# Performance work log

Measured on AMD Instinct MI355X. Metric: run time of the kernel, lower is better.

Reference implementation:

```python
import jax, jax.numpy as jnp
import numpy as np

D_MODEL = 1024
D_FF = 4096
NUM_EXPERTS = 8
NUM_SLOTS = 2
LN_EPS = 1e-5


def setup_inputs() -> dict:
    key = jax.random.key(0)
    ks = jax.random.split(key, 4)
    x = jax.random.normal(ks[0], (4, 4096, D_MODEL), dtype=jnp.float32)
    slot_embeds = jax.random.normal(ks[1], (NUM_EXPERTS * NUM_SLOTS, D_MODEL), dtype=jnp.float32) * 0.02
    # per-expert MLP weights, stacked over expert axis (Linear bias=False)
    W1 = jax.random.normal(ks[2], (NUM_EXPERTS, D_MODEL, D_FF), dtype=jnp.float32) * (1.0 / np.sqrt(D_MODEL))
    W2 = jax.random.normal(ks[3], (NUM_EXPERTS, D_FF, D_MODEL), dtype=jnp.float32) * (1.0 / np.sqrt(D_FF))
    ln_gamma = jnp.ones((D_MODEL,), dtype=jnp.float32)
    ln_beta = jnp.zeros((D_MODEL,), dtype=jnp.float32)
    return {"x": x, "slot_embeds": slot_embeds, "W1": W1, "W2": W2,
            "ln_gamma": ln_gamma, "ln_beta": ln_beta}


def reference(x, slot_embeds, W1, W2, ln_gamma, ln_beta):
    B, T, D = x.shape
    E, S = NUM_EXPERTS, NUM_SLOTS
    # logits: [B, T, E*S]
    logits = jnp.einsum('btd,nd->btn', x, slot_embeds) / jnp.sqrt(jnp.asarray(D, x.dtype))
    # dispatch: softmax over tokens (dim=1)
    dispatch = jax.nn.softmax(logits, axis=1)
    slot_in = jnp.einsum('btn,btd->bnd', dispatch, x)  # [B, E*S, D]
    # LayerNorm over last dim
    mu = jnp.mean(slot_in, axis=-1, keepdims=True)
    var = jnp.mean(jnp.square(slot_in - mu), axis=-1, keepdims=True)
    h = (slot_in - mu) * jax.lax.rsqrt(var + LN_EPS) * ln_gamma + ln_beta
    # per-expert MLP as a single batched (grouped) GEMM pair
    h = h.reshape(B, E, S, D)
    u = jax.nn.gelu(jnp.einsum('besd,edf->besf', h, W1), approximate=False)
    slot_out = jnp.einsum('besf,efd->besd', u, W2).reshape(B, E * S, D)
    # combine: softmax over slots (dim=2)
    combine = jax.nn.softmax(logits, axis=2)
    return jnp.einsum('btn,bnd->btd', combine, slot_out)
```

## Files before the change

### kernel.cpp

```cpp
#include <hip/hip_runtime.h>
#include <math.h>

#define NB 4
#define NT 4096
#define ND 1024
#define NS 16
#define NE 8
#define NF 4096

__device__ __forceinline__ float gelu(float v) {
  return 0.5f * v * (1.f + erff(v * 0.70710678118654752f));
}
__device__ __forceinline__ void fma4(float4& a, float s, const float4& v) {
  a.x += s * v.x; a.y += s * v.y; a.z += s * v.z; a.w += s * v.w;
}
__device__ __forceinline__ float4 ld4(const float* p) {
  return *reinterpret_cast<const float4*>(p);
}

__global__ __launch_bounds__(256, 4) void k_logits(const float* __restrict__ x,
                                                   const float* __restrict__ se,
                                                   float* __restrict__ logits) {
  const int wave = threadIdx.x >> 6, lane = threadIdx.x & 63;
  const int t0 = blockIdx.x * 16 + wave * 4;
  float acc[64];
#pragma unroll
  for (int j = 0; j < 64; ++j) acc[j] = 0.f;
  for (int it = 0; it < 4; ++it) {
    const int d = it * 256 + lane * 4;
    float4 xv[4];
#pragma unroll
    for (int tt = 0; tt < 4; ++tt)
      xv[tt] = ld4(x + (size_t)(t0 + tt) * ND + d);
#pragma unroll
    for (int n = 0; n < NS; ++n) {
      const float4 sv = ld4(se + (size_t)n * ND + d);
#pragma unroll
      for (int tt = 0; tt < 4; ++tt) {
        acc[tt * 16 + n] += xv[tt].x * sv.x + xv[tt].y * sv.y +
                            xv[tt].z * sv.z + xv[tt].w * sv.w;
      }
    }
  }
#pragma unroll
  for (int k = 0; k < 6; ++k) {
    const int dlt = 1 << k;
    const bool hi = (lane & dlt) != 0;
#pragma unroll
    for (int i = 0; i < (64 >> (k + 1)); ++i) {
      const float a = acc[2 * i], b = acc[2 * i + 1];
      const float send = hi ? a : b;
      const float recv = __shfl_xor(send, dlt, 64);
      acc[i] = (hi ? b : a) + recv;
    }
  }
  logits[(size_t)t0 * NS + lane] = acc[0] * 0.03125f;
}

__global__ __launch_bounds__(256) void k_softmax_stats(const float* __restrict__ logits,
                                                       float* __restrict__ stats) {
  int bn = blockIdx.x;
  int b = bn >> 4, n = bn & 15;
  __shared__ float red[256];
  const float* lp = logits + ((size_t)b * NT) * NS + n;
  float m = -1e30f;
  for (int t = threadIdx.x; t < NT; t += 256) m = fmaxf(m, lp[(size_t)t * NS]);
  red[threadIdx.x] = m; __syncthreads();
  for (int s = 128; s > 0; s >>= 1) {
    if (threadIdx.x < s) red[threadIdx.x] = fmaxf(red[threadIdx.x], red[threadIdx.x + s]);
    __syncthreads();
  }
  m = red[0]; __syncthreads();
  float sm = 0.f;
  for (int t = threadIdx.x; t < NT; t += 256) sm += expf(lp[(size_t)t * NS] - m);
  red[threadIdx.x] = sm; __syncthreads();
  for (int s = 128; s > 0; s >>= 1) {
    if (threadIdx.x < s) red[threadIdx.x] += red[threadIdx.x + s];
    __syncthreads();
  }
  if (threadIdx.x == 0) { stats[bn * 2] = m; stats[bn * 2 + 1] = red[0]; }
}

__global__ __launch_bounds__(256) void k_slot_in(const float* __restrict__ x,
                                                 const float* __restrict__ logits,
                                                 const float* __restrict__ stats,
                                                 float* __restrict__ si_part) {
  __shared__ float s_w[NS][64];
  const int tc = blockIdx.x, b = blockIdx.y;
  const int t0 = tc * 64;
  for (int i = threadIdx.x; i < NS * 64; i += 256) {
    const int n = i >> 6, t = i & 63;
    const float m = stats[(b * NS + n) * 2], s1 = stats[(b * NS + n) * 2 + 1];
    s_w[n][t] = expf(logits[((size_t)b * NT + t0 + t) * NS + n] - m) / s1;
  }
  __syncthreads();
  float4 acc[NS];
#pragma unroll
  for (int n = 0; n < NS; ++n) acc[n] = make_float4(0.f, 0.f, 0.f, 0.f);
  const int d = threadIdx.x * 4;
  const float* xb = x + ((size_t)b * NT + t0) * ND + d;
  float4 xv[2][8];
#pragma unroll
  for (int k = 0; k < 8; ++k) xv[0][k] = ld4(xb + (size_t)k * ND);
#pragma unroll
  for (int g = 0; g < 8; ++g) {
    const int cur = g & 1;
    if (g < 7) {
#pragma unroll
      for (int k = 0; k < 8; ++k)
        xv[cur ^ 1][k] = ld4(xb + (size_t)((g + 1) * 8 + k) * ND);
    }
#pragma unroll
    for (int n = 0; n < NS; ++n) {
      const float4 w0 = ld4(&s_w[n][g * 8]);
      const float4 w1 = ld4(&s_w[n][g * 8 + 4]);
      fma4(acc[n], w0.x, xv[cur][0]); fma4(acc[n], w0.y, xv[cur][1]);
      fma4(acc[n], w0.z, xv[cur][2]); fma4(acc[n], w0.w, xv[cur][3]);
      fma4(acc[n], w1.x, xv[cur][4]); fma4(acc[n], w1.y, xv[cur][5]);
      fma4(acc[n], w1.z, xv[cur][6]); fma4(acc[n], w1.w, xv[cur][7]);
    }
  }
#pragma unroll
  for (int n = 0; n < NS; ++n)
    *reinterpret_cast<float4*>(si_part + (((size_t)tc * 4 + b) * NS + n) * ND + d) = acc[n];
}

__global__ __launch_bounds__(256) void k_reduce_si(const float* __restrict__ si_part,
                                                   float* __restrict__ slot_in) {
  const int i = blockIdx.x * 256 + threadIdx.x;
  const int row = i >> 10, d = i & 1023;
  const int b = row >> 4, n = row & 15;
  float sum = 0.f;
  for (int tc = 0; tc < 64; ++tc)
    sum += si_part[(((size_t)tc * 4 + b) * NS + n) * ND + d];
  slot_in[i] = sum;
}

__global__ __launch_bounds__(256) void k_layernorm(float* __restrict__ slot_in,
                                                   const float* __restrict__ gamma,
                                                   const float* __restrict__ beta) {
  int row = blockIdx.x;
  __shared__ float red[256];
  float* rp = slot_in + (size_t)row * ND;
  float v[4];
  float sum = 0.f;
#pragma unroll
  for (int j = 0; j < 4; ++j) { v[j] = rp[threadIdx.x + j * 256]; sum += v[j]; }
  red[threadIdx.x] = sum; __syncthreads();
  for (int s = 128; s > 0; s >>= 1) {
    if (threadIdx.x < s) red[threadIdx.x] += red[threadIdx.x + s];
    __syncthreads();
  }
  float mu = red[0] * (1.f / ND); __syncthreads();
  float vs = 0.f;
#pragma unroll
  for (int j = 0; j < 4; ++j) { float t = v[j] - mu; vs += t * t; }
  red[threadIdx.x] = vs; __syncthreads();
  for (int s = 128; s > 0; s >>= 1) {
    if (threadIdx.x < s) red[threadIdx.x] += red[threadIdx.x + s];
    __syncthreads();
  }
  float rstd = rsqrtf(red[0] * (1.f / ND) + 1e-5f);
#pragma unroll
  for (int j = 0; j < 4; ++j) {
    int dd = threadIdx.x + j * 256;
    rp[dd] = (v[j] - mu) * rstd * gamma[dd] + beta[dd];
  }
}

__global__ __launch_bounds__(512, 4) void k_mlp1(const float* __restrict__ h,
                                                 const float* __restrict__ W1,
                                                 float* __restrict__ u_part) {
  __shared__ float s_h[64][8];
  __shared__ float4 s_red[8][256];
  const int ft = blockIdx.x, dc = blockIdx.y, e = blockIdx.z;
  {
    const int dd = threadIdx.x >> 3, j = threadIdx.x & 7;
    const int b = j >> 1, s = j & 1;
    s_h[dd][j] = h[((size_t)b * NS + e * 2 + s) * ND + dc * 64 + dd];
  }
  __syncthreads();
  const int tid = threadIdx.x & 255, half = threadIdx.x >> 8;
  float4 acc[8];
#pragma unroll
  for (int j = 0; j < 8; ++j) acc[j] = make_float4(0.f, 0.f, 0.f, 0.f);
  const int f = ft * 1024 + tid * 4;
  const float* wb = W1 + ((size_t)e * ND + dc * 64 + half * 32) * NF + f;
  float4 wv[2][4];
#pragma unroll
  for (int k = 0; k < 4; ++k) wv[0][k] = ld4(wb + (size_t)k * NF);
#pragma unroll
  for (int g = 0; g < 8; ++g) {
    const int cur = g & 1;
    if (g < 7) {
#pragma unroll
      for (int k = 0; k < 4; ++k)
        wv[cur ^ 1][k] = ld4(wb + (size_t)((g + 1) * 4 + k) * NF);
    }
#pragma unroll
    for (int k = 0; k < 4; ++k) {
      const int dd = half * 32 + g * 4 + k;
      const float4 h0 = ld4(&s_h[dd][0]);
      const float4 h1 = ld4(&s_h[dd][4]);
      fma4(acc[0], h0.x, wv[cur][k]); fma4(acc[1], h0.y, wv[cur][k]);
      fma4(acc[2], h0.z, wv[cur][k]); fma4(acc[3], h0.w, wv[cur][k]);
      fma4(acc[4], h1.x, wv[cur][k]); fma4(acc[5], h1.y, wv[cur][k]);
      fma4(acc[6], h1.z, wv[cur][k]); fma4(acc[7], h1.w, wv[cur][k]);
    }
  }
  if (half == 1) {
#pragma unroll
    for (int j = 0; j < 8; ++j) s_red[j][tid] = acc[j];
  }
  __syncthreads();
  if (half == 0) {
#pragma unroll
    for (int j = 0; j < 8; ++j) {
      const float4 o = s_red[j][tid];
      acc[j].x += o.x; acc[j].y += o.y; acc[j].z += o.z; acc[j].w += o.w;
      const int b = j >> 1, s = j & 1;
      const size_t row = ((size_t)b * NE + e) * 2 + s;
      *reinterpret_cast<float4*>(u_part + ((size_t)dc * 64 + row) * NF + f) = acc[j];
    }
  }
}

__global__ __launch_bounds__(256) void k_reduce_gelu(const float* __restrict__ u_part,
                                                     float* __restrict__ u) {
  const int i = blockIdx.x * 256 + threadIdx.x;
  float sum = 0.f;
  for (int dc = 0; dc < 16; ++dc)
    sum += u_part[(size_t)dc * 262144 + i];
  u[i] = gelu(sum);
}

__global__ __launch_bounds__(512, 4) void k_mlp2(const float* __restrict__ u,
                                                 const float* __restrict__ W2,
                                                 float* __restrict__ so_part) {
  __shared__ float s_u[64][8];
  __shared__ float4 s_red[8][256];
  const int fc = blockIdx.x, e = blockIdx.y;
  {
    const int ff = threadIdx.x >> 3, j = threadIdx.x & 7;
    const int b = j >> 1, s = j & 1;
    s_u[ff][j] = u[(((size_t)b * NE + e) * 2 + s) * NF + fc * 64 + ff];
  }
  __syncthreads();
  const int tid = threadIdx.x & 255, half = threadIdx.x >> 8;
  float4 acc[8];
#pragma unroll
  for (int j = 0; j < 8; ++j) acc[j] = make_float4(0.f, 0.f, 0.f, 0.f);
  const int d = tid * 4;
  const float* wb = W2 + ((size_t)e * NF + fc * 64 + half * 32) * ND + d;
  float4 wv[2][4];
#pragma unroll
  for (int k = 0; k < 4; ++k) wv[0][k] = ld4(wb + (size_t)k * ND);
#pragma unroll
  for (int g = 0; g < 8; ++g) {
    const int cur = g & 1;
    if (g < 7) {
#pragma unroll
      for (int k = 0; k < 4; ++k)
        wv[cur ^ 1][k] = ld4(wb + (size_t)((g + 1) * 4 + k) * ND);
    }
#pragma unroll
    for (int k = 0; k < 4; ++k) {
      const int ff = half * 32 + g * 4 + k;
      const float4 u0 = ld4(&s_u[ff][0]);
      const float4 u1 = ld4(&s_u[ff][4]);
      fma4(acc[0], u0.x, wv[cur][k]); fma4(acc[1], u0.y, wv[cur][k]);
      fma4(acc[2], u0.z, wv[cur][k]); fma4(acc[3], u0.w, wv[cur][k]);
      fma4(acc[4], u1.x, wv[cur][k]); fma4(acc[5], u1.y, wv[cur][k]);
      fma4(acc[6], u1.z, wv[cur][k]); fma4(acc[7], u1.w, wv[cur][k]);
    }
  }
  if (half == 1) {
#pragma unroll
    for (int j = 0; j < 8; ++j) s_red[j][tid] = acc[j];
  }
  __syncthreads();
  if (half == 0) {
#pragma unroll
    for (int j = 0; j < 8; ++j) {
      const float4 o = s_red[j][tid];
      acc[j].x += o.x; acc[j].y += o.y; acc[j].z += o.z; acc[j].w += o.w;
      const int b = j >> 1, s = j & 1;
      const size_t row = (size_t)b * NS + e * 2 + s;
      *reinterpret_cast<float4*>(so_part + ((size_t)fc * 64 + row) * ND + d) = acc[j];
    }
  }
}

__global__ __launch_bounds__(256) void k_reduce_so(const float* __restrict__ so_part,
                                                   float* __restrict__ slot_out) {
  const int i = blockIdx.x * 256 + threadIdx.x;
  float sum = 0.f;
  for (int fc = 0; fc < 64; ++fc)
    sum += so_part[(size_t)fc * 65536 + i];
  slot_out[i] = sum;
}

__global__ __launch_bounds__(256) void k_combine(const float* __restrict__ logits,
                                                 const float* __restrict__ slot_out,
                                                 float* __restrict__ out) {
  __shared__ float s_so[NS * ND];
  const int tb = blockIdx.x, b = blockIdx.y;
  for (int i = threadIdx.x; i < NS * ND; i += 256)
    s_so[i] = slot_out[(size_t)b * NS * ND + i];
  __syncthreads();
  const int wave = threadIdx.x >> 6, lane = threadIdx.x & 63;
  const int tbase = tb * 64 + wave * 16;
  for (int g = 0; g < 4; ++g) {
    const int t0 = tbase + g * 4;
    float c[4][NS];
#pragma unroll
    for (int tt = 0; tt < 4; ++tt) {
      const float* lp = logits + ((size_t)b * NT + t0 + tt) * NS;
      float l[NS];
      float m = -1e30f;
#pragma unroll
      for (int n = 0; n < NS; ++n) { l[n] = lp[n]; m = fmaxf(m, l[n]); }
      float s = 0.f;
#pragma unroll
      for (int n = 0; n < NS; ++n) { l[n] = expf(l[n] - m); s += l[n]; }
      const float rs = 1.f / s;
#pragma unroll
      for (int n = 0; n < NS; ++n) c[tt][n] = l[n] * rs;
    }
#pragma unroll
    for (int it = 0; it < 4; ++it) {
      const int d = it * 256 + lane * 4;
      float4 acc[4];
#pragma unroll
      for (int tt = 0; tt < 4; ++tt) acc[tt] = make_float4(0.f, 0.f, 0.f, 0.f);
#pragma unroll
      for (int n = 0; n < NS; ++n) {
        const float4 sv = ld4(&s_so[n * ND + d]);
        fma4(acc[0], c[0][n], sv); fma4(acc[1], c[1][n], sv);
        fma4(acc[2], c[2][n], sv); fma4(acc[3], c[3][n], sv);
      }
#pragma unroll
      for (int tt = 0; tt < 4; ++tt)
        *reinterpret_cast<float4*>(out + ((size_t)b * NT + t0 + tt) * ND + d) = acc[tt];
    }
  }
}

extern "C" void kernel_launch(void* const* d_in, const int* in_sizes, int n_in,
                              void* d_out, int out_size, void* d_ws, size_t ws_size,
                              hipStream_t stream) {
  const float* x     = (const float*)d_in[0];
  const float* se    = (const float*)d_in[1];
  const float* W1    = (const float*)d_in[2];
  const float* W2    = (const float*)d_in[3];
  const float* gamma = (const float*)d_in[4];
  const float* beta  = (const float*)d_in[5];
  float* out = (float*)d_out;

  float* ws       = (float*)d_ws;
  float* logits   = ws;
  float* stats    = ws + 262144;
  float* slot_in  = ws + 262400;
  float* slot_out = ws + 327936;
  float* u        = ws + 393472;
  float* si_part  = ws + 655616;
  float* u_part   = ws + 4849920;
  float* so_part  = ws + 9044224;

  k_logits<<<1024, 256, 0, stream>>>(x, se, logits);
  k_softmax_stats<<<NB * NS, 256, 0, stream>>>(logits, stats);
  k_slot_in<<<dim3(64, NB), 256, 0, stream>>>(x, logits, stats, si_part);
  k_reduce_si<<<256, 256, 0, stream>>>(si_part, slot_in);
  k_layernorm<<<NB * NS, 256, 0, stream>>>(slot_in, gamma, beta);
  k_mlp1<<<dim3(4, 16, NE), 512, 0, stream>>>(slot_in, W1, u_part);
  k_reduce_gelu<<<1024, 256, 0, stream>>>(u_part, u);
  k_mlp2<<<dim3(64, NE), 512, 0, stream>>>(u, W2, so_part);
  k_reduce_so<<<256, 256, 0, stream>>>(so_part, slot_out);
  k_combine<<<dim3(64, NB), 256, 0, stream>>>(logits, slot_out, out);
}
```

Measured before the change: 469.1 us.

## Fuse slot reduction with LayerNorm and GELU reduction into MLP2 prologue

Merges the partial slot_in reduction with LayerNorm into a single 1024-thread kernel that uses wave shuffles, removing one launch and a round trip through memory. MLP1 and MLP2 drop their intra-block split-K shared-memory reduction and move to 256-thread blocks over twice as many K-chunks. The separate reduce+GELU kernel is removed, and each MLP2 block now sums the 32 u partials and applies GELU while loading its inputs. In exchange, every MLP2 block rereads u_part, and the so_part partial buffer and its final reduction double in size.

```diff
diff --git a/kernel.cpp b/kernel.cpp
--- a/kernel.cpp
+++ b/kernel.cpp
@@ -125,67 +125,57 @@
     *reinterpret_cast<float4*>(si_part + (((size_t)tc * 4 + b) * NS + n) * ND + d) = acc[n];
 }
 
-__global__ __launch_bounds__(256) void k_reduce_si(const float* __restrict__ si_part,
-                                                   float* __restrict__ slot_in) {
-  const int i = blockIdx.x * 256 + threadIdx.x;
-  const int row = i >> 10, d = i & 1023;
+__global__ __launch_bounds__(1024) void k_reduce_si_ln(const float* __restrict__ si_part,
+                                                       const float* __restrict__ gamma,
+                                                       const float* __restrict__ beta,
+                                                       float* __restrict__ h) {
+  const int row = blockIdx.x;
   const int b = row >> 4, n = row & 15;
-  float sum = 0.f;
+  const int d = threadIdx.x;
+  float v = 0.f;
   for (int tc = 0; tc < 64; ++tc)
-    sum += si_part[(((size_t)tc * 4 + b) * NS + n) * ND + d];
-  slot_in[i] = sum;
-}
-
-__global__ __launch_bounds__(256) void k_layernorm(float* __restrict__ slot_in,
-                                                   const float* __restrict__ gamma,
-                                                   const float* __restrict__ beta) {
-  int row = blockIdx.x;
-  __shared__ float red[256];
-  float* rp = slot_in + (size_t)row * ND;
-  float v[4];
-  float sum = 0.f;
-#pragma unroll
-  for (int j = 0; j < 4; ++j) { v[j] = rp[threadIdx.x + j * 256]; sum += v[j]; }
-  red[threadIdx.x] = sum; __syncthreads();
-  for (int s = 128; s > 0; s >>= 1) {
-    if (threadIdx.x < s) red[threadIdx.x] += red[threadIdx.x + s];
-    __syncthreads();
-  }
-  float mu = red[0] * (1.f / ND); __syncthreads();
-  float vs = 0.f;
-#pragma unroll
-  for (int j = 0; j < 4; ++j) { float t = v[j] - mu; vs += t * t; }
-  red[threadIdx.x] = vs; __syncthreads();
-  for (int s = 128; s > 0; s >>= 1) {
-    if (threadIdx.x < s) red[threadIdx.x] += red[threadIdx.x + s];
-    __syncthreads();
-  }
-  float rstd = rsqrtf(red[0] * (1.f / ND) + 1e-5f);
-#pragma unroll
-  for (int j = 0; j < 4; ++j) {
-    int dd = threadIdx.x + j * 256;
-    rp[dd] = (v[j] - mu) * rstd * gamma[dd] + beta[dd];
-  }
-}
-
-__global__ __launch_bounds__(512, 4) void k_mlp1(const float* __restrict__ h,
+    v += si_part[(((size_t)tc * 4 + b) * NS + n) * ND + d];
+  __shared__ float red[16];
+  float s = v;
+#pragma unroll
+  for (int off = 32; off > 0; off >>= 1) s += __shfl_xor(s, off, 64);
+  if ((threadIdx.x & 63) == 0) red[threadIdx.x >> 6] = s;
+  __syncthreads();
+  float mu = 0.f;
+#pragma unroll
+  for (int w = 0; w < 16; ++w) mu += red[w];
+  mu *= (1.f / ND);
+  __syncthreads();
+  const float q = v - mu;
+  s = q * q;
+#pragma unroll
+  for (int off = 32; off > 0; off >>= 1) s += __shfl_xor(s, off, 64);
+  if ((threadIdx.x & 63) == 0) red[threadIdx.x >> 6] = s;
+  __syncthreads();
+  float var = 0.f;
+#pragma unroll
+  for (int w = 0; w < 16; ++w) var += red[w];
+  var *= (1.f / ND);
+  const float rstd = rsqrtf(var + 1e-5f);
+  h[(size_t)row * ND + d] = q * rstd * gamma[d] + beta[d];
+}
+
+__global__ __launch_bounds__(256, 4) void k_mlp1(const float* __restrict__ h,
                                                  const float* __restrict__ W1,
                                                  float* __restrict__ u_part) {
-  __shared__ float s_h[64][8];
-  __shared__ float4 s_red[8][256];
+  __shared__ float s_h[32][8];
   const int ft = blockIdx.x, dc = blockIdx.y, e = blockIdx.z;
   {
     const int dd = threadIdx.x >> 3, j = threadIdx.x & 7;
     const int b = j >> 1, s = j & 1;
-    s_h[dd][j] = h[((size_t)b * NS + e * 2 + s) * ND + dc * 64 + dd];
-  }
-  __syncthreads();
-  const int tid = threadIdx.x & 255, half = threadIdx.x >> 8;
+    s_h[dd][j] = h[((size_t)b * NS + e * 2 + s) * ND + dc * 32 + dd];
+  }
+  __syncthreads();
   float4 acc[8];
 #pragma unroll
   for (int j = 0; j < 8; ++j) acc[j] = make_float4(0.f, 0.f, 0.f, 0.f);
-  const int f = ft * 1024 + tid * 4;
-  const float* wb = W1 + ((size_t)e * ND + dc * 64 + half * 32) * NF + f;
+  const int f = ft * 1024 + threadIdx.x * 4;
+  const float* wb = W1 + ((size_t)e * ND + dc * 32) * NF + f;
   float4 wv[2][4];
 #pragma unroll
   for (int k = 0; k < 4; ++k) wv[0][k] = ld4(wb + (size_t)k * NF);
@@ -199,7 +189,7 @@
     }
 #pragma unroll
     for (int k = 0; k < 4; ++k) {
-      const int dd = half * 32 + g * 4 + k;
+      const int dd = g * 4 + k;
       const float4 h0 = ld4(&s_h[dd][0]);
       const float4 h1 = ld4(&s_h[dd][4]);
       fma4(acc[0], h0.x, wv[cur][k]); fma4(acc[1], h0.y, wv[cur][k]);
@@ -208,50 +198,34 @@
       fma4(acc[6], h1.z, wv[cur][k]); fma4(acc[7], h1.w, wv[cur][k]);
     }
   }
-  if (half == 1) {
-#pragma unroll
-    for (int j = 0; j < 8; ++j) s_red[j][tid] = acc[j];
-  }
-  __syncthreads();
-  if (half == 0) {
-#pragma unroll
-    for (int j = 0; j < 8; ++j) {
-      const float4 o = s_red[j][tid];
-      acc[j].x += o.x; acc[j].y += o.y; acc[j].z += o.z; acc[j].w += o.w;
-      const int b = j >> 1, s = j & 1;
-      const size_t row = ((size_t)b * NE + e) * 2 + s;
-      *reinterpret_cast<float4*>(u_part + ((size_t)dc * 64 + row) * NF + f) = acc[j];
-    }
-  }
-}
-
-__global__ __launch_bounds__(256) void k_reduce_gelu(const float* __restrict__ u_part,
-                                                     float* __restrict__ u) {
-  const int i = blockIdx.x * 256 + threadIdx.x;
-  float sum = 0.f;
-  for (int dc = 0; dc < 16; ++dc)
-    sum += u_part[(size_t)dc * 262144 + i];
-  u[i] = gelu(sum);
-}
-
-__global__ __launch_bounds__(512, 4) void k_mlp2(const float* __restrict__ u,
+#pragma unroll
+  for (int j = 0; j < 8; ++j) {
+    const int b = j >> 1, s = j & 1;
+    const size_t row = ((size_t)b * NE + e) * 2 + s;
+    *reinterpret_cast<float4*>(u_part + ((size_t)dc * 64 + row) * NF + f) = acc[j];
+  }
+}
+
+__global__ __launch_bounds__(256, 4) void k_mlp2(const float* __restrict__ u_part,
                                                  const float* __restrict__ W2,
                                                  float* __restrict__ so_part) {
-  __shared__ float s_u[64][8];
-  __shared__ float4 s_red[8][256];
+  __shared__ float s_u[32][8];
   const int fc = blockIdx.x, e = blockIdx.y;
   {
-    const int ff = threadIdx.x >> 3, j = threadIdx.x & 7;
+    const int j = threadIdx.x >> 5, ff = threadIdx.x & 31;
     const int b = j >> 1, s = j & 1;
-    s_u[ff][j] = u[(((size_t)b * NE + e) * 2 + s) * NF + fc * 64 + ff];
-  }
-  __syncthreads();
-  const int tid = threadIdx.x & 255, half = threadIdx.x >> 8;
+    const size_t urow = ((size_t)b * NE + e) * 2 + s;
+    float sum = 0.f;
+    for (int dcc = 0; dcc < 32; ++dcc)
+      sum += u_part[((size_t)dcc * 64 + urow) * NF + fc * 32 + ff];
+    s_u[ff][j] = gelu(sum);
+  }
+  __syncthreads();
   float4 acc[8];
 #pragma unroll
   for (int j = 0; j < 8; ++j) acc[j] = make_float4(0.f, 0.f, 0.f, 0.f);
-  const int d = tid * 4;
-  const float* wb = W2 + ((size_t)e * NF + fc * 64 + half * 32) * ND + d;
+  const int d = threadIdx.x * 4;
+  const float* wb = W2 + ((size_t)e * NF + fc * 32) * ND + d;
   float4 wv[2][4];
 #pragma unroll
   for (int k = 0; k < 4; ++k) wv[0][k] = ld4(wb + (size_t)k * ND);
@@ -265,7 +239,7 @@
     }
 #pragma unroll
     for (int k = 0; k < 4; ++k) {
-      const int ff = half * 32 + g * 4 + k;
+      const int ff = g * 4 + k;
       const float4 u0 = ld4(&s_u[ff][0]);
       const float4 u1 = ld4(&s_u[ff][4]);
       fma4(acc[0], u0.x, wv[cur][k]); fma4(acc[1], u0.y, wv[cur][k]);
@@ -274,20 +248,11 @@
       fma4(acc[6], u1.z, wv[cur][k]); fma4(acc[7], u1.w, wv[cur][k]);
     }
   }
-  if (half == 1) {
-#pragma unroll
-    for (int j = 0; j < 8; ++j) s_red[j][tid] = acc[j];
-  }
-  __syncthreads();
-  if (half == 0) {
-#pragma unroll
-    for (int j = 0; j < 8; ++j) {
-      const float4 o = s_red[j][tid];
-      acc[j].x += o.x; acc[j].y += o.y; acc[j].z += o.z; acc[j].w += o.w;
-      const int b = j >> 1, s = j & 1;
-      const size_t row = (size_t)b * NS + e * 2 + s;
-      *reinterpret_cast<float4*>(so_part + ((size_t)fc * 64 + row) * ND + d) = acc[j];
-    }
+#pragma unroll
+  for (int j = 0; j < 8; ++j) {
+    const int b = j >> 1, s = j & 1;
+    const size_t row = (size_t)b * NS + e * 2 + s;
+    *reinterpret_cast<float4*>(so_part + ((size_t)fc * 64 + row) * ND + d) = acc[j];
   }
 }
 
@@ -295,7 +260,7 @@
                                                    float* __restrict__ slot_out) {
   const int i = blockIdx.x * 256 + threadIdx.x;
   float sum = 0.f;
-  for (int fc = 0; fc < 64; ++fc)
+  for (int fc = 0; fc < 128; ++fc)
     sum += so_part[(size_t)fc * 65536 + i];
   slot_out[i] = sum;
 }
@@ -362,19 +327,16 @@
   float* stats    = ws + 262144;
   float* slot_in  = ws + 262400;
   float* slot_out = ws + 327936;
-  float* u        = ws + 393472;
-  float* si_part  = ws + 655616;
-  float* u_part   = ws + 4849920;
-  float* so_part  = ws + 9044224;
+  float* si_part  = ws + 393472;
+  float* u_part   = ws + 4587776;
+  float* so_part  = ws + 12976384;
 
   k_logits<<<1024, 256, 0, stream>>>(x, se, logits);
   k_softmax_stats<<<NB * NS, 256, 0, stream>>>(logits, stats);
   k_slot_in<<<dim3(64, NB), 256, 0, stream>>>(x, logits, stats, si_part);
-  k_reduce_si<<<256, 256, 0, stream>>>(si_part, slot_in);
-  k_layernorm<<<NB * NS, 256, 0, stream>>>(slot_in, gamma, beta);
-  k_mlp1<<<dim3(4, 16, NE), 512, 0, stream>>>(slot_in, W1, u_part);
-  k_reduce_gelu<<<1024, 256, 0, stream>>>(u_part, u);
-  k_mlp2<<<dim3(64, NE), 512, 0, stream>>>(u, W2, so_part);
+  k_reduce_si_ln<<<64, 1024, 0, stream>>>(si_part, gamma, beta, slot_in);
+  k_mlp1<<<dim3(4, 32, NE), 256, 0, stream>>>(slot_in, W1, u_part);
+  k_mlp2<<<dim3(128, NE), 256, 0, stream>>>(u_part, W2, so_part);
   k_reduce_so<<<256, 256, 0, stream>>>(so_part, slot_out);
   k_combine<<<dim3(64, NB), 256, 0, stream>>>(logits, slot_out, out);
 }
```

Result: slower. 480.7 us (+2.5%).

## Fuse split-K reduce+GELU into MLP2, drop intra-block split, use nontemporal weight loads

Applied to the files above, without the earlier changes.

Removes the separate reduce-GELU kernel by having each MLP2 block sum the 16 partial MLP1 outputs for its 64-wide f chunk and apply GELU while staging into shared memory. Both MLP kernels drop the two-half intra-block K split and its shared-memory reduction, running 256 threads that each cover the full 64-row chunk with deeper 8-row double-buffered loads. Weight loads become nontemporal so streamed W1/W2 data bypasses cache retention. The cost is fewer threads per block and redundant partial-sum reads across MLP2 blocks.

```diff
diff --git a/kernel.cpp b/kernel.cpp
--- a/kernel.cpp
+++ b/kernel.cpp
@@ -8,6 +8,8 @@
 #define NE 8
 #define NF 4096
 
+typedef float f32x4 __attribute__((ext_vector_type(4)));
+
 __device__ __forceinline__ float gelu(float v) {
   return 0.5f * v * (1.f + erff(v * 0.70710678118654752f));
 }
@@ -16,6 +18,10 @@
 }
 __device__ __forceinline__ float4 ld4(const float* p) {
   return *reinterpret_cast<const float4*>(p);
+}
+__device__ __forceinline__ float4 ld4nt(const float* p) {
+  f32x4 v = __builtin_nontemporal_load(reinterpret_cast<const f32x4*>(p));
+  return make_float4(v[0], v[1], v[2], v[3]);
 }
 
 __global__ __launch_bounds__(256, 4) void k_logits(const float* __restrict__ x,
@@ -168,38 +174,36 @@
   }
 }
 
-__global__ __launch_bounds__(512, 4) void k_mlp1(const float* __restrict__ h,
-                                                 const float* __restrict__ W1,
-                                                 float* __restrict__ u_part) {
+__global__ __launch_bounds__(256) void k_mlp1(const float* __restrict__ h,
+                                              const float* __restrict__ W1,
+                                              float* __restrict__ u_part) {
   __shared__ float s_h[64][8];
-  __shared__ float4 s_red[8][256];
   const int ft = blockIdx.x, dc = blockIdx.y, e = blockIdx.z;
-  {
-    const int dd = threadIdx.x >> 3, j = threadIdx.x & 7;
+  for (int i = threadIdx.x; i < 512; i += 256) {
+    const int dd = i >> 3, j = i & 7;
     const int b = j >> 1, s = j & 1;
     s_h[dd][j] = h[((size_t)b * NS + e * 2 + s) * ND + dc * 64 + dd];
   }
   __syncthreads();
-  const int tid = threadIdx.x & 255, half = threadIdx.x >> 8;
   float4 acc[8];
 #pragma unroll
   for (int j = 0; j < 8; ++j) acc[j] = make_float4(0.f, 0.f, 0.f, 0.f);
-  const int f = ft * 1024 + tid * 4;
-  const float* wb = W1 + ((size_t)e * ND + dc * 64 + half * 32) * NF + f;
-  float4 wv[2][4];
-#pragma unroll
-  for (int k = 0; k < 4; ++k) wv[0][k] = ld4(wb + (size_t)k * NF);
+  const int f = ft * 1024 + threadIdx.x * 4;
+  const float* wb = W1 + ((size_t)e * ND + dc * 64) * NF + f;
+  float4 wv[2][8];
+#pragma unroll
+  for (int k = 0; k < 8; ++k) wv[0][k] = ld4nt(wb + (size_t)k * NF);
 #pragma unroll
   for (int g = 0; g < 8; ++g) {
     const int cur = g & 1;
     if (g < 7) {
 #pragma unroll
-      for (int k = 0; k < 4; ++k)
-        wv[cur ^ 1][k] = ld4(wb + (size_t)((g + 1) * 4 + k) * NF);
-    }
-#pragma unroll
-    for (int k = 0; k < 4; ++k) {
-      const int dd = half * 32 + g * 4 + k;
+      for (int k = 0; k < 8; ++k)
+        wv[cur ^ 1][k] = ld4nt(wb + (size_t)((g + 1) * 8 + k) * NF);
+    }
+#pragma unroll
+    for (int k = 0; k < 8; ++k) {
+      const int dd = g * 8 + k;
       const float4 h0 = ld4(&s_h[dd][0]);
       const float4 h1 = ld4(&s_h[dd][4]);
       fma4(acc[0], h0.x, wv[cur][k]); fma4(acc[1], h0.y, wv[cur][k]);
@@ -208,64 +212,48 @@
       fma4(acc[6], h1.z, wv[cur][k]); fma4(acc[7], h1.w, wv[cur][k]);
     }
   }
-  if (half == 1) {
-#pragma unroll
-    for (int j = 0; j < 8; ++j) s_red[j][tid] = acc[j];
+#pragma unroll
+  for (int j = 0; j < 8; ++j) {
+    const int b = j >> 1, s = j & 1;
+    const size_t row = ((size_t)b * NE + e) * 2 + s;
+    *reinterpret_cast<float4*>(u_part + ((size_t)dc * 64 + row) * NF + f) = acc[j];
+  }
+}
+
+__global__ __launch_bounds__(256) void k_mlp2(const float* __restrict__ u_part,
+                                              const float* __restrict__ W2,
+                                              float* __restrict__ so_part) {
+  __shared__ float s_u[64][8];
+  const int fc = blockIdx.x, e = blockIdx.y;
+  for (int i = threadIdx.x; i < 512; i += 256) {
+    const int j = i >> 6, ff = i & 63;
+    const int b = j >> 1, s = j & 1;
+    const size_t urow = ((size_t)b * NE + e) * 2 + s;
+    float sum = 0.f;
+    for (int dcc = 0; dcc < 16; ++dcc)
+      sum += u_part[((size_t)dcc * 64 + urow) * NF + fc * 64 + ff];
+    s_u[ff][j] = gelu(sum);
   }
   __syncthreads();
-  if (half == 0) {
-#pragma unroll
-    for (int j = 0; j < 8; ++j) {
-      const float4 o = s_red[j][tid];
-      acc[j].x += o.x; acc[j].y += o.y; acc[j].z += o.z; acc[j].w += o.w;
-      const int b = j >> 1, s = j & 1;
-      const size_t row = ((size_t)b * NE + e) * 2 + s;
-      *reinterpret_cast<float4*>(u_part + ((size_t)dc * 64 + row) * NF + f) = acc[j];
-    }
-  }
-}
-
-__global__ __launch_bounds__(256) void k_reduce_gelu(const float* __restrict__ u_part,
-                                                     float* __restrict__ u) {
-  const int i = blockIdx.x * 256 + threadIdx.x;
-  float sum = 0.f;
-  for (int dc = 0; dc < 16; ++dc)
-    sum += u_part[(size_t)dc * 262144 + i];
-  u[i] = gelu(sum);
-}
-
-__global__ __launch_bounds__(512, 4) void k_mlp2(const float* __restrict__ u,
-                                                 const float* __restrict__ W2,
-                                                 float* __restrict__ so_part) {
-  __shared__ float s_u[64][8];
-  __shared__ float4 s_red[8][256];
-  const int fc = blockIdx.x, e = blockIdx.y;
-  {
-    const int ff = threadIdx.x >> 3, j = threadIdx.x & 7;
-    const int b = j >> 1, s = j & 1;
-    s_u[ff][j] = u[(((size_t)b * NE + e) * 2 + s) * NF + fc * 64 + ff];
-  }
-  __syncthreads();
-  const int tid = threadIdx.x & 255, half = threadIdx.x >> 8;
   float4 acc[8];
 #pragma unroll
   for (int j = 0; j < 8; ++j) acc[j] = make_float4(0.f, 0.f, 0.f, 0.f);
-  const int d = tid * 4;
-  const float* wb = W2 + ((size_t)e * NF + fc * 64 + half * 32) * ND + d;
-  float4 wv[2][4];
-#pragma unroll
-  for (int k = 0; k < 4; ++k) wv[0][k] = ld4(wb + (size_t)k * ND);
+  const int d = threadIdx.x * 4;
+  const float* wb = W2 + ((size_t)e * NF + fc * 64) * ND + d;
+  float4 wv[2][8];
+#pragma unroll
+  for (int k = 0; k < 8; ++k) wv[0][k] = ld4nt(wb + (size_t)k * ND);
 #pragma unroll
   for (int g = 0; g < 8; ++g) {
     const int cur = g & 1;
     if (g < 7) {
 #pragma unroll
-      for (int k = 0; k < 4; ++k)
-        wv[cur ^ 1][k] = ld4(wb + (size_t)((g + 1) * 4 + k) * ND);
-    }
-#pragma unroll
-    for (int k = 0; k < 4; ++k) {
-      const int ff = half * 32 + g * 4 + k;
+      for (int k = 0; k < 8; ++k)
+        wv[cur ^ 1][k] = ld4nt(wb + (size_t)((g + 1) * 8 + k) * ND);
+    }
+#pragma unroll
+    for (int k = 0; k < 8; ++k) {
+      const int ff = g * 8 + k;
       const float4 u0 = ld4(&s_u[ff][0]);
       const float4 u1 = ld4(&s_u[ff][4]);
       fma4(acc[0], u0.x, wv[cur][k]); fma4(acc[1], u0.y, wv[cur][k]);
@@ -274,20 +262,11 @@
       fma4(acc[6], u1.z, wv[cur][k]); fma4(acc[7], u1.w, wv[cur][k]);
     }
   }
-  if (half == 1) {
-#pragma unroll
-    for (int j = 0; j < 8; ++j) s_red[j][tid] = acc[j];
-  }
-  __syncthreads();
-  if (half == 0) {
-#pragma unroll
-    for (int j = 0; j < 8; ++j) {
-      const float4 o = s_red[j][tid];
-      acc[j].x += o.x; acc[j].y += o.y; acc[j].z += o.z; acc[j].w += o.w;
-      const int b = j >> 1, s = j & 1;
-      const size_t row = (size_t)b * NS + e * 2 + s;
-      *reinterpret_cast<float4*>(so_part + ((size_t)fc * 64 + row) * ND + d) = acc[j];
-    }
+#pragma unroll
+  for (int j = 0; j < 8; ++j) {
+    const int b = j >> 1, s = j & 1;
+    const size_t row = (size_t)b * NS + e * 2 + s;
+    *reinterpret_cast<float4*>(so_part + ((size_t)fc * 64 + row) * ND + d) = acc[j];
   }
 }
 
@@ -362,19 +341,17 @@
   float* stats    = ws + 262144;
   float* slot_in  = ws + 262400;
   float* slot_out = ws + 327936;
-  float* u        = ws + 393472;
-  float* si_part  = ws + 655616;
-  float* u_part   = ws + 4849920;
-  float* so_part  = ws + 9044224;
+  float* si_part  = ws + 393472;
+  float* u_part   = ws + 4587776;
+  float* so_part  = ws + 8782080;
 
   k_logits<<<1024, 256, 0, stream>>>(x, se, logits);
   k_softmax_stats<<<NB * NS, 256, 0, stream>>>(logits, stats);
   k_slot_in<<<dim3(64, NB), 256, 0, stream>>>(x, logits, stats, si_part);
   k_reduce_si<<<256, 256, 0, stream>>>(si_part, slot_in);
   k_layernorm<<<NB * NS, 256, 0, stream>>>(slot_in, gamma, beta);
-  k_mlp1<<<dim3(4, 16, NE), 512, 0, stream>>>(slot_in, W1, u_part);
-  k_reduce_gelu<<<1024, 256, 0, stream>>>(u_part, u);
-  k_mlp2<<<dim3(64, NE), 512, 0, stream>>>(u, W2, so_part);
+  k_mlp1<<<dim3(4, 16, NE), 256, 0, stream>>>(slot_in, W1, u_part);
+  k_mlp2<<<dim3(64, NE), 256, 0, stream>>>(u_part, W2, so_part);
   k_reduce_so<<<256, 256, 0, stream>>>(so_part, slot_out);
   k_combine<<<dim3(64, NB), 256, 0, stream>>>(logits, slot_out, out);
 }
```

New measurement: 448.2 us. 4.4% less time.
